# Performance work log

Measured on AMD Instinct MI355X. Metric: run time of the kernel, lower is better.

Reference implementation:

```python
import jax, jax.numpy as jnp
from jax import lax
import numpy as np

B, H, W = 16, 512, 512
OPENING_R, EROSION_R, DILATION_R = 5, 2, 1
MIN_SIZE, AREA_THRESHOLD = 2000, 300
INF = np.int32(2 ** 30)


def _disk(r):
    # skimage.morphology.disk: x^2 + y^2 <= r^2 on a (2r+1)^2 grid
    y, x = np.mgrid[-r:r + 1, -r:r + 1]
    return jnp.asarray((x * x + y * y <= r * r).astype(np.float32))


D_OPEN, D_ERODE, D_DILATE = _disk(OPENING_R), _disk(EROSION_R), _disk(DILATION_R)


def _conv2(x, k):
    return lax.conv_general_dilated(x[None, None], k[None, None], (1, 1), 'VALID')[0, 0]


def _erode(fg, se):
    # skimage binary_erosion uses border_value=True (image border does not erode)
    r = se.shape[0] // 2
    x = jnp.pad(fg.astype(jnp.float32), r, constant_values=1.0)
    return _conv2(x, se) >= se.sum() - 0.5


def _dilate(fg, se):
    # skimage binary_dilation uses border_value=False
    r = se.shape[0] // 2
    x = jnp.pad(fg.astype(jnp.float32), r, constant_values=0.0)
    return _conv2(x, se) > 0.5


def _seg_cummin(v, reset, axis, reverse):
    # segmented cumulative-min: scan resets wherever `reset` is True (background)
    def comb(a, b):
        av, af = a
        bv, bf = b
        return jnp.where(bf, bv, jnp.minimum(av, bv)), af | bf

    vv, _ = lax.associative_scan(comb, (v, reset), axis=axis, reverse=reverse)
    return vv


def _label(fg):
    # 4-connectivity connected-component labeling via min-label propagation.
    # Each fg pixel starts with its raveled index; alternating row/col segmented
    # cummin sweeps run under while_loop until a fixed point (root id per comp).
    h, w = fg.shape
    idx = jnp.arange(h * w, dtype=jnp.int32).reshape(h, w)
    lab0 = jnp.where(fg, idx, INF)
    bg = ~fg

    def sweep(l):
        for axis in (1, 0):
            for rev in (False, True):
                l = jnp.where(fg, _seg_cummin(l, bg, axis, rev), INF)
        return l

    def body(c):
        l, _ = c
        nl = sweep(l)
        return nl, jnp.array_equal(nl, l)

    lab, _ = lax.while_loop(lambda c: ~c[1], body, (lab0, jnp.array(False)))
    seg = jnp.where(fg, lab, 0).ravel()
    sizes = jax.ops.segment_sum(fg.astype(jnp.int32).ravel(), seg, num_segments=h * w)
    ncomp = jnp.sum(sizes > 0)
    return lab, sizes, ncomp


def _remove_small_objects(fg, min_size, guard):
    lab, sizes, ncomp = _label(fg)
    px = sizes[jnp.where(fg, lab, 0)]  # component size at every fg pixel
    kept = fg & (px >= min_size)
    # original only removes small objects when label(...).max() > 1
    return jnp.where(ncomp > 1, kept, fg) if guard else kept


def _pipeline(mask):
    fg = mask > 0
    fg = _remove_small_objects(fg, MIN_SIZE, True)
    # remove_small_holes == ~remove_small_objects(~fg, area_threshold + 1)
    fg = ~_remove_small_objects(~fg, AREA_THRESHOLD + 1, False)
    fg = _erode(fg, D_ERODE)
    fg = _dilate(_erode(fg, D_OPEN), D_OPEN)  # binary_opening
    fg = _remove_small_objects(fg, MIN_SIZE, True)
    fg = _dilate(fg, D_DILATE)
    return fg.astype(jnp.float32)  # original casts to int; float32 kept for vjp parity


def setup_inputs() -> dict:
    key = jax.random.key(0)
    # blobby binary masks: threshold bilinearly-upsampled low-res noise so that
    # realistic large connected components (> min_size px) exist
    low = jax.random.uniform(key, (B, H // 16, W // 16), dtype=jnp.float32)
    blob = jax.image.resize(low, (B, H, W), method='bilinear')
    return {'inputs': (blob > 0.5).astype(jnp.float32)}


def reference(inputs):
    return jax.vmap(_pipeline)(inputs)
```

## Files before the change

kernel.cpp:

```cpp
#include <hip/hip_runtime.h>
#include <stdint.h>

#define BATCH 16
#define H 512
#define W 512
#define HW (H * W)
#define NTOT (BATCH * HW)
#define NWORDS (NTOT / 64)

#define SROWS 16
#define SWORDS 128
#define SPIX 8192
#define NSTRIPS (NWORDS / SWORDS)
#define IMG_STRIPS 32
#define NBOUND_IMG 248

#define MAXR 4096
#define NR (NSTRIPS * MAXR)

#define SPIN_LIMIT (1 << 20)

__device__ __forceinline__ int ald(const int* p) {
    return __hip_atomic_load((int*)p, __ATOMIC_RELAXED, __HIP_MEMORY_SCOPE_AGENT);
}
__device__ __forceinline__ void ast(int* p, int v) {
    __hip_atomic_store(p, v, __ATOMIC_RELAXED, __HIP_MEMORY_SCOPE_AGENT);
}
__device__ __forceinline__ uint64_t ald64(const uint64_t* p) {
    return __hip_atomic_load((uint64_t*)p, __ATOMIC_RELAXED, __HIP_MEMORY_SCOPE_AGENT);
}
__device__ __forceinline__ void ast64(uint64_t* p, uint64_t v) {
    __hip_atomic_store(p, v, __ATOMIC_RELAXED, __HIP_MEMORY_SCOPE_AGENT);
}

__device__ __forceinline__ int find_root_c(int* L, int x) {
    int r = x, p = ald(&L[r]);
    while (p != r) { r = p; p = ald(&L[r]); }
    if (ald(&L[x]) != r) atomicMin(&L[x], r);
    return r;
}

__device__ void merge_uf(int* L, int a, int b) {
    while (true) {
        a = find_root_c(L, a);
        b = find_root_c(L, b);
        if (a == b) return;
        int lo = a < b ? a : b;
        int hi = a < b ? b : a;
        int old = atomicMin(&L[hi], lo);
        if (old == hi) return;
        a = lo; b = old;
    }
}

__device__ __forceinline__ int find_root_lds(int* P, int x) {
    int r = x, p = P[r];
    while (p != r) { r = p; p = P[r]; }
    return r;
}

__device__ void merge_lds(int* P, int a, int b) {
    while (true) {
        a = find_root_lds(P, a);
        b = find_root_lds(P, b);
        if (a == b) return;
        int lo = a < b ? a : b;
        int hi = a < b ? b : a;
        int old = atomicMin(&P[hi], lo);
        if (old == hi) return;
        a = lo; b = old;
    }
}

__device__ __forceinline__ int run_of(uint64_t m, int i, int cvrid, int wr) {
    uint64_t below = i ? ((~m) & ((1ull << i) - 1)) : 0ull;
    if (below == 0) return (cvrid >= 0) ? cvrid : wr;
    int s = 64 - __builtin_clzll(below);
    uint64_t starts = m & ~((m << 1) | ((cvrid >= 0) ? 1ull : 0ull));
    return wr + __popcll(starts & ((1ull << s) - 1));
}

__device__ __forceinline__ int run_of_lds(uint64_t m, int i, int cvrid,
                                          uint64_t starts, int wb) {
    uint64_t below = i ? ((~m) & ((1ull << i) - 1)) : 0ull;
    if (below == 0) return (cvrid >= 0) ? cvrid : wb;
    int s = 64 - __builtin_clzll(below);
    return wb + __popcll(starts & ((1ull << s) - 1));
}

__device__ uint64_t keep_word(const uint64_t* __restrict__ bits,
                              const int* __restrict__ carry, const int* __restrict__ wordrun,
                              const int* __restrict__ L, const int* __restrict__ sizes,
                              const int* __restrict__ ncomp, int minsz, int gw) {
    uint64_t m = ald64(&bits[gw]);
    uint64_t res = m;
    if (m && ald(&ncomp[gw >> 12]) > 1) {
        int cv = ald(&carry[gw]);
        int wr = ald(&wordrun[gw]);
        int rk = 0;
        while (m) {
            int s = __builtin_ctzll(m);
            uint64_t rest = m >> s;
            uint64_t nr = ~rest;
            int len = nr ? __builtin_ctzll(nr) : (64 - s);
            uint64_t piece = ((len >= 64) ? ~0ull : ((1ull << len) - 1)) << s;
            bool initial = !(s == 0 && cv >= 0);
            int rid = initial ? (wr + rk++) : cv;
            if (ald(&sizes[ald(&L[rid])]) < minsz) res &= ~piece;
            m &= ~piece;
        }
    }
    return res;
}

__device__ uint64_t fill_word(const uint64_t* __restrict__ bits,
                              const int* __restrict__ carry, const int* __restrict__ wordrun,
                              const int* __restrict__ L, const int* __restrict__ sizes,
                              int minsz, int gw) {
    uint64_t fg = ald64(&bits[gw]);
    uint64_t bg = ~fg;
    uint64_t res = fg;
    int cv = ald(&carry[gw]);
    int wr = ald(&wordrun[gw]);
    int rk = 0;
    while (bg) {
        int s = __builtin_ctzll(bg);
        uint64_t rest = bg >> s;
        uint64_t nr = ~rest;
        int len = nr ? __builtin_ctzll(nr) : (64 - s);
        uint64_t piece = ((len >= 64) ? ~0ull : ((1ull << len) - 1)) << s;
        bool initial = !(s == 0 && cv >= 0);
        int rid = initial ? (wr + rk++) : cv;
        if (ald(&sizes[ald(&L[rid])]) < minsz) res |= piece;
        bg &= ~piece;
    }
    return res;
}

template <int R, bool ERODE>
__device__ uint64_t morph_word_lds(const uint64_t* buf, int lrow, int w, int gyTop) {
    const uint64_t BORDER = ERODE ? ~0ull : 0ull;
    uint64_t res = ERODE ? ~0ull : 0ull;
#pragma unroll
    for (int dy = -R; dy <= R; ++dy) {
        int lr = lrow + dy;
        int gy = gyTop + lr;
        if (gy < 0 || gy >= H) continue;
        int v = R * R - dy * dy;
        int kx = 0;
        while ((kx + 1) * (kx + 1) <= v) ++kx;
        uint64_t cur = buf[lr * 8 + w];
        uint64_t prv = (w > 0) ? buf[lr * 8 + w - 1] : BORDER;
        uint64_t nxt = (w < 7) ? buf[lr * 8 + w + 1] : BORDER;
        uint64_t acc = cur;
#pragma unroll
        for (int dx = 1; dx <= kx; ++dx) {
            uint64_t right = (cur >> dx) | (nxt << (64 - dx));
            uint64_t left  = (cur << dx) | (prv >> (64 - dx));
            if (ERODE) acc &= right & left;
            else       acc |= right | left;
        }
        if (ERODE) res &= acc;
        else       res |= acc;
    }
    return res;
}

__device__ void strip_ccl_body(uint64_t m, uint64_t* sw, int* scarry,
                               int* cntL, int* wbL, int* par,
                               int blk, int t,
                               int* __restrict__ carry, int* __restrict__ wordrun,
                               int* __restrict__ L, int* __restrict__ sizes,
                               int* __restrict__ ncomp) {
    if (t < SWORDS) sw[t] = m;
    __syncthreads();

    if (t < SWORDS) {
        bool cont = (t & 7) ? ((sw[t - 1] >> 63) != 0) : false;
        int c = __popcll(m & ~(m << 1));
        if ((m & 1ull) && cont) --c;
        cntL[t] = c;
        wbL[t] = c;
    }
    __syncthreads();
    for (int off = 1; off < SWORDS; off <<= 1) {
        int v = 0;
        if (t < SWORDS && t >= off) v = wbL[t - off];
        __syncthreads();
        if (t < SWORDS) wbL[t] += v;
        __syncthreads();
    }

    if (t < SROWS) {
        int cv = -1;
        for (int i = 0; i < 8; ++i) {
            int lw = t * 8 + i;
            scarry[lw] = cv;
            uint64_t w = sw[lw];
            if (w >> 63) { if (cntL[lw] > 0) cv = wbL[lw] - 1; }
            else cv = -1;
        }
    }
    for (int i = t; i < MAXR; i += 256) par[i] = i;
    __syncthreads();

    int cv = -1, wb = 0;
    uint64_t starts = 0ull;
    if (t < SWORDS) {
        cv = scarry[t];
        wb = wbL[t] - cntL[t];
        ast(&carry[blk * SWORDS + t], (cv >= 0) ? (blk * MAXR + cv) : -1);
        ast(&wordrun[blk * SWORDS + t], blk * MAXR + wb);
        starts = m & ~((m << 1) | ((cv >= 0) ? 1ull : 0ull));
    }
    __syncthreads();

    if (t >= 8 && t < SWORDS && m) {
        uint64_t up = sw[t - 8];
        uint64_t cand = m & up;
        if (cand) {
            uint64_t curprev = (t & 7) ? sw[t - 1] : 0ull;
            uint64_t upprev  = (t & 7) ? sw[t - 9] : 0ull;
            uint64_t curl = (m << 1) | (curprev >> 63);
            uint64_t upl  = (up << 1) | (upprev >> 63);
            cand &= ~(curl & upl);
            int cvu = scarry[t - 8];
            int wbu = wbL[t - 8] - cntL[t - 8];
            uint64_t startsU = up & ~((up << 1) | ((cvu >= 0) ? 1ull : 0ull));
            while (cand) {
                int i = __builtin_ctzll(cand);
                int sP = run_of_lds(m, i, cv, starts, wb);
                int sQ = run_of_lds(up, i, cvu, startsU, wbu);
                merge_lds(par, sP, sQ);
                cand &= cand - 1;
            }
        }
    }
    __syncthreads();

    if (t < SWORDS) {
        int g = blk * MAXR;
        uint64_t ss = starts;
        int rk = 0;
        while (ss) {
            int rid = wb + rk; ++rk;
            int r = find_root_lds(par, rid);
            ast(&L[g + rid], g + r);
            if (r == rid) ast(&sizes[g + rid], 0);
            ss &= ss - 1;
        }
    }
    if (t == 0 && (blk & 31) == 0) ast(&ncomp[blk >> 5], 0);
}

__device__ void merge_bound_item(const uint64_t* __restrict__ bits, uint64_t inv64,
                                 const int* __restrict__ carry,
                                 const int* __restrict__ wordrun,
                                 int* __restrict__ L, int gw, int w) {
    uint64_t cur = ald64(&bits[gw]) ^ inv64;
    uint64_t up  = ald64(&bits[gw - 8]) ^ inv64;
    uint64_t cand = cur & up;
    if (!cand) return;
    uint64_t curprev = w ? (ald64(&bits[gw - 1]) ^ inv64) : 0ull;
    uint64_t upprev  = w ? (ald64(&bits[gw - 9]) ^ inv64) : 0ull;
    uint64_t curl = (cur << 1) | (curprev >> 63);
    uint64_t upl  = (up << 1)  | (upprev >> 63);
    cand &= ~(curl & upl);
    if (!cand) return;
    int cvc = ald(&carry[gw]), cvu = ald(&carry[gw - 8]);
    int wrc = ald(&wordrun[gw]), wru = ald(&wordrun[gw - 8]);
    while (cand) {
        int i = __builtin_ctzll(cand);
        int sP = run_of(cur, i, cvc, wrc);
        int sQ = run_of(up, i, cvu, wru);
        merge_uf(L, sP, sQ);
        cand &= cand - 1;
    }
}

__device__ void flatten_block(const uint64_t* __restrict__ bits, uint64_t inv64,
                              const int* __restrict__ carry,
                              const int* __restrict__ wordrun,
                              int* __restrict__ L,
                              int* __restrict__ sizes, int* __restrict__ ncomp,
                              int blk, int t, int* hk, int* hv) {
    if (t < 128) { hk[t] = -1; hv[t] = 0; }
    __syncthreads();
    if (t < SWORDS) {
        int gw = blk * SWORDS + t;
        uint64_t m = ald64(&bits[gw]) ^ inv64;
        if (m) {
            int cv = ald(&carry[gw]);
            int wr = ald(&wordrun[gw]);
            int rk = 0;
            while (m) {
                int s = __builtin_ctzll(m);
                uint64_t rest = m >> s;
                uint64_t nr = ~rest;
                int len = nr ? __builtin_ctzll(nr) : (64 - s);
                uint64_t piece = ((len >= 64) ? ~0ull : ((1ull << len) - 1)) << s;
                bool initial = !(s == 0 && cv >= 0);
                int rid = initial ? (wr + rk++) : cv;
                int r = find_root_c(L, rid);
                if (initial && r == rid) atomicAdd(&ncomp[gw >> 12], 1);
                int cnt = __popcll(piece);
                uint32_t h = ((uint32_t)r * 2654435761u) >> 25;
                bool done = false;
                for (int tt = 0; tt < 16; ++tt) {
                    int slot = (h + tt) & 127;
                    int k = hk[slot];
                    if (k == -1) k = atomicCAS(&hk[slot], -1, r);
                    if (k == -1 || k == r) { atomicAdd(&hv[slot], cnt); done = true; break; }
                }
                if (!done) atomicAdd(&sizes[r], cnt);
                m &= ~piece;
            }
        }
    }
    __syncthreads();
    if (t < 128 && hk[t] != -1) atomicAdd(&sizes[hk[t]], hv[t]);
}

__device__ void keep_dilate_seg(const uint64_t* __restrict__ bits,
                                const int* __restrict__ carry,
                                const int* __restrict__ wordrun,
                                const int* __restrict__ L,
                                const int* __restrict__ sizes,
                                const int* __restrict__ ncomp,
                                float* __restrict__ out,
                                int img, int y0, int t, uint64_t* kb, uint64_t* db) {
    if (t < 80) {
        int lr = t >> 3;
        int w = t & 7;
        int gy = y0 - 1 + lr;
        uint64_t v = 0;
        if (gy >= 0 && gy < H)
            v = keep_word(bits, carry, wordrun, L, sizes, ncomp, 2000,
                          img * 4096 + gy * 8 + w);
        kb[t] = v;
    }
    __syncthreads();
    if (t < 64) {
        int r = t >> 3, w = t & 7;
        uint64_t cur = kb[(r + 1) * 8 + w];
        uint64_t up  = kb[r * 8 + w];
        uint64_t dn  = kb[(r + 2) * 8 + w];
        uint64_t prv = w ? kb[(r + 1) * 8 + w - 1] : 0ull;
        uint64_t nxt = (w < 7) ? kb[(r + 1) * 8 + w + 1] : 0ull;
        db[t] = cur | up | dn | (cur << 1) | (prv >> 63) | (cur >> 1) | (nxt << 63);
    }
    __syncthreads();

    int q0 = t * 16;
    uint64_t wd = db[q0 >> 6];
    int sh = q0 & 63;
    float4* o = (float4*)(out + (size_t)img * HW + (size_t)y0 * W + q0);
#pragma unroll
    for (int k = 0; k < 4; ++k) {
        uint32_t nib = (uint32_t)(wd >> (sh + k * 4)) & 0xFu;
        float4 f;
        f.x = (nib & 1u) ? 1.0f : 0.0f;
        f.y = (nib & 2u) ? 1.0f : 0.0f;
        f.z = (nib & 4u) ? 1.0f : 0.0f;
        f.w = (nib & 8u) ? 1.0f : 0.0f;
        o[k] = f;
    }
}

__device__ __forceinline__ void ibar(int* flags, int img, int si, int phase) {
    int* base = flags + img * 32;
    __syncthreads();
    if (threadIdx.x == 0) {
        asm volatile("s_waitcnt vmcnt(0)" ::: "memory");
        ast(&base[si], phase);
    }
    if (threadIdx.x < 32) {
        int spins = 0;
        while (ald(&base[threadIdx.x]) < phase && ++spins < SPIN_LIMIT)
            __builtin_amdgcn_s_sleep(1);
    }
    __syncthreads();
}

__global__ __launch_bounds__(256, 2) void k_mega(
        const float4* __restrict__ in4, float* __restrict__ out,
        int* LA, int* sizesA, int* LB, int* sizesB,
        uint64_t* bits1, uint64_t* bits2, uint64_t* bits3,
        int* carryA, int* carryB, int* wordrunA, int* wordrunB,
        int* ncompA, int* ncompB, int* flags) {
    __shared__ uint64_t sw[SWORDS];
    __shared__ int scarry[SWORDS];
    __shared__ int cntL[SWORDS];
    __shared__ int wbL[SWORDS];
    __shared__ union US {
        int par[MAXR];
        struct { uint64_t A[320]; uint64_t B[320]; } mo;
        struct { int hk[128]; int hv[128]; } ha;
        struct { uint64_t kb[80]; uint64_t db[64]; } kd;
    } U;
    int blk = blockIdx.x;
    int t = threadIdx.x;
    int img = blk >> 5, si = blk & 31;

#pragma unroll
    for (int it = 0; it < 8; ++it) {
        int q = blk * (SPIX / 4) + it * 256 + t;
        float4 v = in4[q];
        uint32_t nib = (v.x > 0.0f ? 1u : 0u) | (v.y > 0.0f ? 2u : 0u) |
                       (v.z > 0.0f ? 4u : 0u) | (v.w > 0.0f ? 8u : 0u);
        uint64_t val = (uint64_t)nib << (4 * (t & 15));
        val |= __shfl_xor(val, 1);
        val |= __shfl_xor(val, 2);
        val |= __shfl_xor(val, 4);
        val |= __shfl_xor(val, 8);
        if ((t & 15) == 0) ast64(&bits1[q >> 4], val);
    }
    __syncthreads();

    {
        uint64_t m = (t < SWORDS) ? ald64(&bits1[blk * SWORDS + t]) : 0ull;
        strip_ccl_body(m, sw, scarry, cntL, wbL, U.par, blk, t,
                       carryA, wordrunA, LA, sizesA, ncompA);
    }
    ibar(flags, img, si, 1);

    if (t < 8) {
        int item = si * 8 + t;
        if (item < NBOUND_IMG) {
            int gw = img * 4096 + ((item >> 3) + 1) * SROWS * 8 + (item & 7);
            merge_bound_item(bits1, 0ull, carryA, wordrunA, LA, gw, item & 7);
        }
    }
    ibar(flags, img, si, 2);

    flatten_block(bits1, 0ull, carryA, wordrunA, LA, sizesA, ncompA,
                  blk, t, U.ha.hk, U.ha.hv);
    ibar(flags, img, si, 3);

    {
        uint64_t m = 0ull;
        if (t < SWORDS) {
            int gw = blk * SWORDS + t;
            uint64_t kw = keep_word(bits1, carryA, wordrunA, LA, sizesA, ncompA,
                                    2000, gw);
            ast64(&bits2[gw], kw);
            m = ~kw;
        }
        strip_ccl_body(m, sw, scarry, cntL, wbL, U.par, blk, t,
                       carryB, wordrunB, LB, sizesB, ncompB);
    }
    ibar(flags, img, si, 4);

    if (t < 8) {
        int item = si * 8 + t;
        if (item < NBOUND_IMG) {
            int gw = img * 4096 + ((item >> 3) + 1) * SROWS * 8 + (item & 7);
            merge_bound_item(bits2, ~0ull, carryB, wordrunB, LB, gw, item & 7);
        }
    }
    ibar(flags, img, si, 5);

    flatten_block(bits2, ~0ull, carryB, wordrunB, LB, sizesB, ncompB,
                  blk, t, U.ha.hk, U.ha.hv);
    ibar(flags, img, si, 6);

    {
        int gyTop = si * 16 - 12;
        for (int lw = t; lw < 320; lw += 256) {
            int gy = gyTop + (lw >> 3);
            int w = lw & 7;
            uint64_t v = 0;
            if (gy >= 0 && gy < H)
                v = fill_word(bits2, carryB, wordrunB, LB, sizesB, 301,
                              img * 4096 + gy * 8 + w);
            U.mo.A[lw] = v;
        }
        __syncthreads();
        for (int lw = t; lw < 320; lw += 256) {
            int lr = lw >> 3;
            if (lr >= 2 && lr <= 37) U.mo.B[lw] = morph_word_lds<2, true>(U.mo.A, lr, lw & 7, gyTop);
        }
        __syncthreads();
        for (int lw = t; lw < 320; lw += 256) {
            int lr = lw >> 3;
            if (lr >= 7 && lr <= 32) U.mo.A[lw] = morph_word_lds<5, true>(U.mo.B, lr, lw & 7, gyTop);
        }
        __syncthreads();
        for (int lw = t; lw < 320; lw += 256) {
            int lr = lw >> 3;
            if (lr >= 12 && lr <= 27) U.mo.B[lw] = morph_word_lds<5, false>(U.mo.A, lr, lw & 7, gyTop);
        }
        __syncthreads();
        uint64_t m3 = 0ull;
        if (t < SWORDS) {
            m3 = U.mo.B[t + 96];
            ast64(&bits3[blk * SWORDS + t], m3);
        }
        strip_ccl_body(m3, sw, scarry, cntL, wbL, U.par, blk, t,
                       carryA, wordrunA, LA, sizesA, ncompA);
    }
    ibar(flags, img, si, 7);

    if (t < 8) {
        int item = si * 8 + t;
        if (item < NBOUND_IMG) {
            int gw = img * 4096 + ((item >> 3) + 1) * SROWS * 8 + (item & 7);
            merge_bound_item(bits3, 0ull, carryA, wordrunA, LA, gw, item & 7);
        }
    }
    ibar(flags, img, si, 8);

    flatten_block(bits3, 0ull, carryA, wordrunA, LA, sizesA, ncompA,
                  blk, t, U.ha.hk, U.ha.hv);
    ibar(flags, img, si, 9);

    for (int k = 0; k < 2; ++k) {
        int seg = blk * 2 + k;
        int s8 = seg & 63;
        keep_dilate_seg(bits3, carryA, wordrunA, LA, sizesA, ncompA, out,
                        img, s8 * 8, t, U.kd.kb, U.kd.db);
        __syncthreads();
    }
}

extern "C" void kernel_launch(void* const* d_in, const int* in_sizes, int n_in,
                              void* d_out, int out_size, void* d_ws, size_t ws_size,
                              hipStream_t stream) {
    const float* in = (const float*)d_in[0];
    float* out = (float*)d_out;

    uint8_t* ws = (uint8_t*)d_ws;
    int* LA      = (int*)ws;
    int* sizesA  = LA + NR;
    int* LB      = sizesA + NR;
    int* sizesB  = LB + NR;
    uint64_t* bits1 = (uint64_t*)(sizesB + NR);
    uint64_t* bits2 = bits1 + NWORDS;
    uint64_t* bits3 = bits2 + NWORDS;
    int* carryA   = (int*)(bits3 + NWORDS);
    int* carryB   = carryA + NWORDS;
    int* wordrunA = carryB + NWORDS;
    int* wordrunB = wordrunA + NWORDS;
    int* ncompA   = wordrunB + NWORDS;
    int* ncompB   = ncompA + BATCH;
    int* flags    = ncompB + BATCH;

    hipMemsetAsync(flags, 0, BATCH * 32 * sizeof(int), stream);

    k_mega<<<NSTRIPS, 256, 0, stream>>>((const float4*)in, out,
                                        LA, sizesA, LB, sizesB,
                                        bits1, bits2, bits3,
                                        carryA, carryB, wordrunA, wordrunB,
                                        ncompA, ncompB, flags);
}
```

Before: 186.9 us.

## Reuse strip-local LDS CCL state, batch label lookups, and drop flag memset via epochs

Boundary merge, flatten, keep and fill steps now read the strip's own words, carries and run bases from shared memory instead of reloading them from global memory. Root and size lookups for the first four runs of each word are issued together to expose memory-level parallelism. The per-launch memset of the barrier flags is replaced by a persistent device array with epoch-relative phases, removing one extra launch. This relies on the shared-memory state still holding the matching stage's data at each step, and it makes the barrier flags grow monotonically across calls.

```diff
diff --git a/kernel.cpp b/kernel.cpp
--- a/kernel.cpp
+++ b/kernel.cpp
@@ -13,12 +13,13 @@
 #define SPIX 8192
 #define NSTRIPS (NWORDS / SWORDS)
 #define IMG_STRIPS 32
-#define NBOUND_IMG 248
 
 #define MAXR 4096
 #define NR (NSTRIPS * MAXR)
 
 #define SPIN_LIMIT (1 << 20)
+
+__device__ int g_flags[BATCH * 32];
 
 __device__ __forceinline__ int ald(const int* p) {
     return __hip_atomic_load((int*)p, __ATOMIC_RELAXED, __HIP_MEMORY_SCOPE_AGENT);
@@ -88,53 +89,179 @@
     return wb + __popcll(starts & ((1ull << s) - 1));
 }
 
-__device__ uint64_t keep_word(const uint64_t* __restrict__ bits,
-                              const int* __restrict__ carry, const int* __restrict__ wordrun,
-                              const int* __restrict__ L, const int* __restrict__ sizes,
-                              const int* __restrict__ ncomp, int minsz, int gw) {
-    uint64_t m = ald64(&bits[gw]);
+__device__ __forceinline__ void hash_add(int* hk, int* hv, int* sizes,
+                                         int r, int cnt) {
+    uint32_t h = ((uint32_t)r * 2654435761u) >> 25;
+    for (int tt = 0; tt < 16; ++tt) {
+        int slot = (h + tt) & 127;
+        int k = hk[slot];
+        if (k == -1) k = atomicCAS(&hk[slot], -1, r);
+        if (k == -1 || k == r) { atomicAdd(&hv[slot], cnt); return; }
+    }
+    atomicAdd(&sizes[r], cnt);
+}
+
+__device__ uint64_t keep_core(uint64_t m, int cvg, int wrg, int nc,
+                              const int* L, const int* sizes, int minsz) {
     uint64_t res = m;
-    if (m && ald(&ncomp[gw >> 12]) > 1) {
-        int cv = ald(&carry[gw]);
-        int wr = ald(&wordrun[gw]);
-        int rk = 0;
-        while (m) {
-            int s = __builtin_ctzll(m);
-            uint64_t rest = m >> s;
+    if (!m) return res;
+    uint64_t rem = m;
+    uint64_t pc[4]; int rd[4];
+    int rk = 0;
+#pragma unroll
+    for (int k = 0; k < 4; ++k) {
+        pc[k] = 0; rd[k] = wrg;
+        if (rem) {
+            int s = __builtin_ctzll(rem);
+            uint64_t rest = rem >> s;
             uint64_t nr = ~rest;
             int len = nr ? __builtin_ctzll(nr) : (64 - s);
             uint64_t piece = ((len >= 64) ? ~0ull : ((1ull << len) - 1)) << s;
-            bool initial = !(s == 0 && cv >= 0);
-            int rid = initial ? (wr + rk++) : cv;
+            bool initial = !(s == 0 && cvg >= 0);
+            pc[k] = piece;
+            rd[k] = initial ? (wrg + rk) : cvg;
+            rk += initial ? 1 : 0;
+            rem &= ~piece;
+        }
+    }
+    int rt[4], sz[4];
+#pragma unroll
+    for (int k = 0; k < 4; ++k) rt[k] = ald(&L[rd[k]]);
+#pragma unroll
+    for (int k = 0; k < 4; ++k) {
+        int idx = pc[k] ? rt[k] : rd[k];
+        sz[k] = ald(&sizes[idx]);
+    }
+    if (nc > 1) {
+#pragma unroll
+        for (int k = 0; k < 4; ++k)
+            if (pc[k] && sz[k] < minsz) res &= ~pc[k];
+        while (rem) {
+            int s = __builtin_ctzll(rem);
+            uint64_t rest = rem >> s;
+            uint64_t nr = ~rest;
+            int len = nr ? __builtin_ctzll(nr) : (64 - s);
+            uint64_t piece = ((len >= 64) ? ~0ull : ((1ull << len) - 1)) << s;
+            int rid = wrg + rk++;
             if (ald(&sizes[ald(&L[rid])]) < minsz) res &= ~piece;
-            m &= ~piece;
+            rem &= ~piece;
         }
     }
     return res;
 }
 
-__device__ uint64_t fill_word(const uint64_t* __restrict__ bits,
-                              const int* __restrict__ carry, const int* __restrict__ wordrun,
-                              const int* __restrict__ L, const int* __restrict__ sizes,
-                              int minsz, int gw) {
-    uint64_t fg = ald64(&bits[gw]);
+__device__ uint64_t fill_core(uint64_t fg, int cvg, int wrg,
+                              const int* L, const int* sizes, int minsz) {
     uint64_t bg = ~fg;
     uint64_t res = fg;
-    int cv = ald(&carry[gw]);
-    int wr = ald(&wordrun[gw]);
+    if (!bg) return res;
+    uint64_t rem = bg;
+    uint64_t pc[4]; int rd[4];
     int rk = 0;
-    while (bg) {
-        int s = __builtin_ctzll(bg);
-        uint64_t rest = bg >> s;
+#pragma unroll
+    for (int k = 0; k < 4; ++k) {
+        pc[k] = 0; rd[k] = wrg;
+        if (rem) {
+            int s = __builtin_ctzll(rem);
+            uint64_t rest = rem >> s;
+            uint64_t nr = ~rest;
+            int len = nr ? __builtin_ctzll(nr) : (64 - s);
+            uint64_t piece = ((len >= 64) ? ~0ull : ((1ull << len) - 1)) << s;
+            bool initial = !(s == 0 && cvg >= 0);
+            pc[k] = piece;
+            rd[k] = initial ? (wrg + rk) : cvg;
+            rk += initial ? 1 : 0;
+            rem &= ~piece;
+        }
+    }
+    int rt[4], sz[4];
+#pragma unroll
+    for (int k = 0; k < 4; ++k) rt[k] = ald(&L[rd[k]]);
+#pragma unroll
+    for (int k = 0; k < 4; ++k) {
+        int idx = pc[k] ? rt[k] : rd[k];
+        sz[k] = ald(&sizes[idx]);
+    }
+#pragma unroll
+    for (int k = 0; k < 4; ++k)
+        if (pc[k] && sz[k] < minsz) res |= pc[k];
+    while (rem) {
+        int s = __builtin_ctzll(rem);
+        uint64_t rest = rem >> s;
         uint64_t nr = ~rest;
         int len = nr ? __builtin_ctzll(nr) : (64 - s);
         uint64_t piece = ((len >= 64) ? ~0ull : ((1ull << len) - 1)) << s;
-        bool initial = !(s == 0 && cv >= 0);
-        int rid = initial ? (wr + rk++) : cv;
+        int rid = wrg + rk++;
         if (ald(&sizes[ald(&L[rid])]) < minsz) res |= piece;
-        bg &= ~piece;
+        rem &= ~piece;
     }
     return res;
+}
+
+__device__ void flatten_fast(uint64_t m, int cvg, int wrg,
+                             int* L, int* sizes, int* ncomp_img,
+                             int t, int* hk, int* hv) {
+    if (t < 128) { hk[t] = -1; hv[t] = 0; }
+    __syncthreads();
+    if (t < SWORDS && m) {
+        uint64_t rem = m;
+        uint64_t pc[4]; int rd[4]; bool ini[4];
+        int rk = 0;
+#pragma unroll
+        for (int k = 0; k < 4; ++k) {
+            pc[k] = 0; rd[k] = wrg; ini[k] = false;
+            if (rem) {
+                int s = __builtin_ctzll(rem);
+                uint64_t rest = rem >> s;
+                uint64_t nr = ~rest;
+                int len = nr ? __builtin_ctzll(nr) : (64 - s);
+                uint64_t piece = ((len >= 64) ? ~0ull : ((1ull << len) - 1)) << s;
+                bool initial = !(s == 0 && cvg >= 0);
+                pc[k] = piece;
+                rd[k] = initial ? (wrg + rk) : cvg;
+                ini[k] = initial;
+                rk += initial ? 1 : 0;
+                rem &= ~piece;
+            }
+        }
+        int h1[4], h2[4];
+#pragma unroll
+        for (int k = 0; k < 4; ++k) h1[k] = ald(&L[rd[k]]);
+#pragma unroll
+        for (int k = 0; k < 4; ++k) {
+            int i1 = pc[k] ? h1[k] : rd[k];
+            h2[k] = ald(&L[i1]);
+        }
+#pragma unroll
+        for (int k = 0; k < 4; ++k) {
+            if (pc[k]) {
+                int r;
+                if (h2[k] == h1[k]) r = h1[k];
+                else {
+                    r = h2[k];
+                    int p = ald(&L[r]);
+                    while (p != r) { r = p; p = ald(&L[r]); }
+                }
+                if (h1[k] != r) atomicMin(&L[rd[k]], r);
+                if (ini[k] && r == rd[k]) atomicAdd(ncomp_img, 1);
+                hash_add(hk, hv, sizes, r, __popcll(pc[k]));
+            }
+        }
+        while (rem) {
+            int s = __builtin_ctzll(rem);
+            uint64_t rest = rem >> s;
+            uint64_t nr = ~rest;
+            int len = nr ? __builtin_ctzll(nr) : (64 - s);
+            uint64_t piece = ((len >= 64) ? ~0ull : ((1ull << len) - 1)) << s;
+            int rid = wrg + rk++;
+            int r = find_root_c(L, rid);
+            if (r == rid) atomicAdd(ncomp_img, 1);
+            hash_add(hk, hv, sizes, r, __popcll(piece));
+            rem &= ~piece;
+        }
+    }
+    __syncthreads();
+    if (t < 128 && hk[t] != -1) atomicAdd(&sizes[hk[t]], hv[t]);
 }
 
 template <int R, bool ERODE>
@@ -253,130 +380,16 @@
     if (t == 0 && (blk & 31) == 0) ast(&ncomp[blk >> 5], 0);
 }
 
-__device__ void merge_bound_item(const uint64_t* __restrict__ bits, uint64_t inv64,
-                                 const int* __restrict__ carry,
-                                 const int* __restrict__ wordrun,
-                                 int* __restrict__ L, int gw, int w) {
-    uint64_t cur = ald64(&bits[gw]) ^ inv64;
-    uint64_t up  = ald64(&bits[gw - 8]) ^ inv64;
-    uint64_t cand = cur & up;
-    if (!cand) return;
-    uint64_t curprev = w ? (ald64(&bits[gw - 1]) ^ inv64) : 0ull;
-    uint64_t upprev  = w ? (ald64(&bits[gw - 9]) ^ inv64) : 0ull;
-    uint64_t curl = (cur << 1) | (curprev >> 63);
-    uint64_t upl  = (up << 1)  | (upprev >> 63);
-    cand &= ~(curl & upl);
-    if (!cand) return;
-    int cvc = ald(&carry[gw]), cvu = ald(&carry[gw - 8]);
-    int wrc = ald(&wordrun[gw]), wru = ald(&wordrun[gw - 8]);
-    while (cand) {
-        int i = __builtin_ctzll(cand);
-        int sP = run_of(cur, i, cvc, wrc);
-        int sQ = run_of(up, i, cvu, wru);
-        merge_uf(L, sP, sQ);
-        cand &= cand - 1;
-    }
-}
-
-__device__ void flatten_block(const uint64_t* __restrict__ bits, uint64_t inv64,
-                              const int* __restrict__ carry,
-                              const int* __restrict__ wordrun,
-                              int* __restrict__ L,
-                              int* __restrict__ sizes, int* __restrict__ ncomp,
-                              int blk, int t, int* hk, int* hv) {
-    if (t < 128) { hk[t] = -1; hv[t] = 0; }
-    __syncthreads();
-    if (t < SWORDS) {
-        int gw = blk * SWORDS + t;
-        uint64_t m = ald64(&bits[gw]) ^ inv64;
-        if (m) {
-            int cv = ald(&carry[gw]);
-            int wr = ald(&wordrun[gw]);
-            int rk = 0;
-            while (m) {
-                int s = __builtin_ctzll(m);
-                uint64_t rest = m >> s;
-                uint64_t nr = ~rest;
-                int len = nr ? __builtin_ctzll(nr) : (64 - s);
-                uint64_t piece = ((len >= 64) ? ~0ull : ((1ull << len) - 1)) << s;
-                bool initial = !(s == 0 && cv >= 0);
-                int rid = initial ? (wr + rk++) : cv;
-                int r = find_root_c(L, rid);
-                if (initial && r == rid) atomicAdd(&ncomp[gw >> 12], 1);
-                int cnt = __popcll(piece);
-                uint32_t h = ((uint32_t)r * 2654435761u) >> 25;
-                bool done = false;
-                for (int tt = 0; tt < 16; ++tt) {
-                    int slot = (h + tt) & 127;
-                    int k = hk[slot];
-                    if (k == -1) k = atomicCAS(&hk[slot], -1, r);
-                    if (k == -1 || k == r) { atomicAdd(&hv[slot], cnt); done = true; break; }
-                }
-                if (!done) atomicAdd(&sizes[r], cnt);
-                m &= ~piece;
-            }
-        }
-    }
-    __syncthreads();
-    if (t < 128 && hk[t] != -1) atomicAdd(&sizes[hk[t]], hv[t]);
-}
-
-__device__ void keep_dilate_seg(const uint64_t* __restrict__ bits,
-                                const int* __restrict__ carry,
-                                const int* __restrict__ wordrun,
-                                const int* __restrict__ L,
-                                const int* __restrict__ sizes,
-                                const int* __restrict__ ncomp,
-                                float* __restrict__ out,
-                                int img, int y0, int t, uint64_t* kb, uint64_t* db) {
-    if (t < 80) {
-        int lr = t >> 3;
-        int w = t & 7;
-        int gy = y0 - 1 + lr;
-        uint64_t v = 0;
-        if (gy >= 0 && gy < H)
-            v = keep_word(bits, carry, wordrun, L, sizes, ncomp, 2000,
-                          img * 4096 + gy * 8 + w);
-        kb[t] = v;
-    }
-    __syncthreads();
-    if (t < 64) {
-        int r = t >> 3, w = t & 7;
-        uint64_t cur = kb[(r + 1) * 8 + w];
-        uint64_t up  = kb[r * 8 + w];
-        uint64_t dn  = kb[(r + 2) * 8 + w];
-        uint64_t prv = w ? kb[(r + 1) * 8 + w - 1] : 0ull;
-        uint64_t nxt = (w < 7) ? kb[(r + 1) * 8 + w + 1] : 0ull;
-        db[t] = cur | up | dn | (cur << 1) | (prv >> 63) | (cur >> 1) | (nxt << 63);
-    }
-    __syncthreads();
-
-    int q0 = t * 16;
-    uint64_t wd = db[q0 >> 6];
-    int sh = q0 & 63;
-    float4* o = (float4*)(out + (size_t)img * HW + (size_t)y0 * W + q0);
-#pragma unroll
-    for (int k = 0; k < 4; ++k) {
-        uint32_t nib = (uint32_t)(wd >> (sh + k * 4)) & 0xFu;
-        float4 f;
-        f.x = (nib & 1u) ? 1.0f : 0.0f;
-        f.y = (nib & 2u) ? 1.0f : 0.0f;
-        f.z = (nib & 4u) ? 1.0f : 0.0f;
-        f.w = (nib & 8u) ? 1.0f : 0.0f;
-        o[k] = f;
-    }
-}
-
-__device__ __forceinline__ void ibar(int* flags, int img, int si, int phase) {
-    int* base = flags + img * 32;
+__device__ __forceinline__ void ibar(int img, int si, int ep, int phase) {
+    int* base = g_flags + img * 32;
     __syncthreads();
     if (threadIdx.x == 0) {
         asm volatile("s_waitcnt vmcnt(0)" ::: "memory");
-        ast(&base[si], phase);
+        ast(&base[si], ep + phase);
     }
     if (threadIdx.x < 32) {
         int spins = 0;
-        while (ald(&base[threadIdx.x]) < phase && ++spins < SPIN_LIMIT)
+        while (ald(&base[threadIdx.x]) - ep < phase && ++spins < SPIN_LIMIT)
             __builtin_amdgcn_s_sleep(1);
     }
     __syncthreads();
@@ -387,7 +400,7 @@
         int* LA, int* sizesA, int* LB, int* sizesB,
         uint64_t* bits1, uint64_t* bits2, uint64_t* bits3,
         int* carryA, int* carryB, int* wordrunA, int* wordrunB,
-        int* ncompA, int* ncompB, int* flags) {
+        int* ncompA, int* ncompB) {
     __shared__ uint64_t sw[SWORDS];
     __shared__ int scarry[SWORDS];
     __shared__ int cntL[SWORDS];
@@ -401,6 +414,7 @@
     int blk = blockIdx.x;
     int t = threadIdx.x;
     int img = blk >> 5, si = blk & 31;
+    int ep = ald(&g_flags[img * 32 + si]);
 
 #pragma unroll
     for (int it = 0; it < 8; ++it) {
@@ -413,56 +427,108 @@
         val |= __shfl_xor(val, 2);
         val |= __shfl_xor(val, 4);
         val |= __shfl_xor(val, 8);
-        if ((t & 15) == 0) ast64(&bits1[q >> 4], val);
+        if ((t & 15) == 0) {
+            ast64(&bits1[q >> 4], val);
+            sw[it * 16 + (t >> 4)] = val;
+        }
     }
     __syncthreads();
 
     {
-        uint64_t m = (t < SWORDS) ? ald64(&bits1[blk * SWORDS + t]) : 0ull;
+        uint64_t m = (t < SWORDS) ? sw[t] : 0ull;
         strip_ccl_body(m, sw, scarry, cntL, wbL, U.par, blk, t,
                        carryA, wordrunA, LA, sizesA, ncompA);
     }
-    ibar(flags, img, si, 1);
-
-    if (t < 8) {
-        int item = si * 8 + t;
-        if (item < NBOUND_IMG) {
-            int gw = img * 4096 + ((item >> 3) + 1) * SROWS * 8 + (item & 7);
-            merge_bound_item(bits1, 0ull, carryA, wordrunA, LA, gw, item & 7);
-        }
-    }
-    ibar(flags, img, si, 2);
-
-    flatten_block(bits1, 0ull, carryA, wordrunA, LA, sizesA, ncompA,
-                  blk, t, U.ha.hk, U.ha.hv);
-    ibar(flags, img, si, 3);
+    ibar(img, si, ep, 1);
+
+    if (t < 8 && si < 31) {
+        int gw = (blk + 1) * SWORDS + t;
+        uint64_t cur = ald64(&bits1[gw]);
+        uint64_t curprev = t ? ald64(&bits1[gw - 1]) : 0ull;
+        int cvc = ald(&carryA[gw]);
+        int wrc = ald(&wordrunA[gw]);
+        uint64_t up = sw[120 + t];
+        uint64_t upprev = t ? sw[119 + t] : 0ull;
+        int cvuL = scarry[120 + t];
+        int cvu = cvuL >= 0 ? blk * MAXR + cvuL : -1;
+        int wru = blk * MAXR + (wbL[120 + t] - cntL[120 + t]);
+        uint64_t cand = cur & up;
+        if (cand) {
+            uint64_t curl = (cur << 1) | (curprev >> 63);
+            uint64_t upl  = (up << 1) | (upprev >> 63);
+            cand &= ~(curl & upl);
+            while (cand) {
+                int i = __builtin_ctzll(cand);
+                int sP = run_of(cur, i, cvc, wrc);
+                int sQ = run_of(up, i, cvu, wru);
+                merge_uf(LA, sP, sQ);
+                cand &= cand - 1;
+            }
+        }
+    }
+    ibar(img, si, ep, 2);
 
     {
-        uint64_t m = 0ull;
+        uint64_t m = (t < SWORDS) ? sw[t] : 0ull;
+        int cvL = (t < SWORDS) ? scarry[t] : -1;
+        int cvg = cvL >= 0 ? blk * MAXR + cvL : -1;
+        int wrg = blk * MAXR + ((t < SWORDS) ? (wbL[t] - cntL[t]) : 0);
+        flatten_fast(m, cvg, wrg, LA, sizesA, &ncompA[img], t, U.ha.hk, U.ha.hv);
+    }
+    ibar(img, si, ep, 3);
+
+    {
+        uint64_t m2 = 0ull;
         if (t < SWORDS) {
-            int gw = blk * SWORDS + t;
-            uint64_t kw = keep_word(bits1, carryA, wordrunA, LA, sizesA, ncompA,
-                                    2000, gw);
-            ast64(&bits2[gw], kw);
-            m = ~kw;
-        }
-        strip_ccl_body(m, sw, scarry, cntL, wbL, U.par, blk, t,
+            int nc = ald(&ncompA[img]);
+            uint64_t m1 = sw[t];
+            int cvL = scarry[t];
+            int cvg = cvL >= 0 ? blk * MAXR + cvL : -1;
+            int wrg = blk * MAXR + (wbL[t] - cntL[t]);
+            uint64_t kw = keep_core(m1, cvg, wrg, nc, LA, sizesA, 2000);
+            ast64(&bits2[blk * SWORDS + t], kw);
+            m2 = ~kw;
+        }
+        strip_ccl_body(m2, sw, scarry, cntL, wbL, U.par, blk, t,
                        carryB, wordrunB, LB, sizesB, ncompB);
     }
-    ibar(flags, img, si, 4);
-
-    if (t < 8) {
-        int item = si * 8 + t;
-        if (item < NBOUND_IMG) {
-            int gw = img * 4096 + ((item >> 3) + 1) * SROWS * 8 + (item & 7);
-            merge_bound_item(bits2, ~0ull, carryB, wordrunB, LB, gw, item & 7);
-        }
-    }
-    ibar(flags, img, si, 5);
-
-    flatten_block(bits2, ~0ull, carryB, wordrunB, LB, sizesB, ncompB,
-                  blk, t, U.ha.hk, U.ha.hv);
-    ibar(flags, img, si, 6);
+    ibar(img, si, ep, 4);
+
+    if (t < 8 && si < 31) {
+        int gw = (blk + 1) * SWORDS + t;
+        uint64_t cur = ~ald64(&bits2[gw]);
+        uint64_t curprev = t ? ~ald64(&bits2[gw - 1]) : 0ull;
+        int cvc = ald(&carryB[gw]);
+        int wrc = ald(&wordrunB[gw]);
+        uint64_t up = sw[120 + t];
+        uint64_t upprev = t ? sw[119 + t] : 0ull;
+        int cvuL = scarry[120 + t];
+        int cvu = cvuL >= 0 ? blk * MAXR + cvuL : -1;
+        int wru = blk * MAXR + (wbL[120 + t] - cntL[120 + t]);
+        uint64_t cand = cur & up;
+        if (cand) {
+            uint64_t curl = (cur << 1) | (curprev >> 63);
+            uint64_t upl  = (up << 1) | (upprev >> 63);
+            cand &= ~(curl & upl);
+            while (cand) {
+                int i = __builtin_ctzll(cand);
+                int sP = run_of(cur, i, cvc, wrc);
+                int sQ = run_of(up, i, cvu, wru);
+                merge_uf(LB, sP, sQ);
+                cand &= cand - 1;
+            }
+        }
+    }
+    ibar(img, si, ep, 5);
+
+    {
+        uint64_t m = (t < SWORDS) ? sw[t] : 0ull;
+        int cvL = (t < SWORDS) ? scarry[t] : -1;
+        int cvg = cvL >= 0 ? blk * MAXR + cvL : -1;
+        int wrg = blk * MAXR + ((t < SWORDS) ? (wbL[t] - cntL[t]) : 0);
+        flatten_fast(m, cvg, wrg, LB, sizesB, &ncompB[img], t, U.ha.hk, U.ha.hv);
+    }
+    ibar(img, si, ep, 6);
 
     {
         int gyTop = si * 16 - 12;
@@ -470,9 +536,22 @@
             int gy = gyTop + (lw >> 3);
             int w = lw & 7;
             uint64_t v = 0;
-            if (gy >= 0 && gy < H)
-                v = fill_word(bits2, carryB, wordrunB, LB, sizesB, 301,
-                              img * 4096 + gy * 8 + w);
+            if (gy >= 0 && gy < H) {
+                uint64_t fg; int cvg, wrg;
+                if (lw >= 96 && lw < 224) {
+                    int ti = lw - 96;
+                    fg = ~sw[ti];
+                    int cvL = scarry[ti];
+                    cvg = cvL >= 0 ? blk * MAXR + cvL : -1;
+                    wrg = blk * MAXR + (wbL[ti] - cntL[ti]);
+                } else {
+                    int gw = img * 4096 + gy * 8 + w;
+                    fg = ald64(&bits2[gw]);
+                    cvg = ald(&carryB[gw]);
+                    wrg = ald(&wordrunB[gw]);
+                }
+                v = fill_core(fg, cvg, wrg, LB, sizesB, 301);
+            }
             U.mo.A[lw] = v;
         }
         __syncthreads();
@@ -499,26 +578,99 @@
         strip_ccl_body(m3, sw, scarry, cntL, wbL, U.par, blk, t,
                        carryA, wordrunA, LA, sizesA, ncompA);
     }
-    ibar(flags, img, si, 7);
-
-    if (t < 8) {
-        int item = si * 8 + t;
-        if (item < NBOUND_IMG) {
-            int gw = img * 4096 + ((item >> 3) + 1) * SROWS * 8 + (item & 7);
-            merge_bound_item(bits3, 0ull, carryA, wordrunA, LA, gw, item & 7);
-        }
-    }
-    ibar(flags, img, si, 8);
-
-    flatten_block(bits3, 0ull, carryA, wordrunA, LA, sizesA, ncompA,
-                  blk, t, U.ha.hk, U.ha.hv);
-    ibar(flags, img, si, 9);
+    ibar(img, si, ep, 7);
+
+    if (t < 8 && si < 31) {
+        int gw = (blk + 1) * SWORDS + t;
+        uint64_t cur = ald64(&bits3[gw]);
+        uint64_t curprev = t ? ald64(&bits3[gw - 1]) : 0ull;
+        int cvc = ald(&carryA[gw]);
+        int wrc = ald(&wordrunA[gw]);
+        uint64_t up = sw[120 + t];
+        uint64_t upprev = t ? sw[119 + t] : 0ull;
+        int cvuL = scarry[120 + t];
+        int cvu = cvuL >= 0 ? blk * MAXR + cvuL : -1;
+        int wru = blk * MAXR + (wbL[120 + t] - cntL[120 + t]);
+        uint64_t cand = cur & up;
+        if (cand) {
+            uint64_t curl = (cur << 1) | (curprev >> 63);
+            uint64_t upl  = (up << 1) | (upprev >> 63);
+            cand &= ~(curl & upl);
+            while (cand) {
+                int i = __builtin_ctzll(cand);
+                int sP = run_of(cur, i, cvc, wrc);
+                int sQ = run_of(up, i, cvu, wru);
+                merge_uf(LA, sP, sQ);
+                cand &= cand - 1;
+            }
+        }
+    }
+    ibar(img, si, ep, 8);
+
+    {
+        uint64_t m = (t < SWORDS) ? sw[t] : 0ull;
+        int cvL = (t < SWORDS) ? scarry[t] : -1;
+        int cvg = cvL >= 0 ? blk * MAXR + cvL : -1;
+        int wrg = blk * MAXR + ((t < SWORDS) ? (wbL[t] - cntL[t]) : 0);
+        flatten_fast(m, cvg, wrg, LA, sizesA, &ncompA[img], t, U.ha.hk, U.ha.hv);
+    }
+    ibar(img, si, ep, 9);
 
     for (int k = 0; k < 2; ++k) {
-        int seg = blk * 2 + k;
-        int s8 = seg & 63;
-        keep_dilate_seg(bits3, carryA, wordrunA, LA, sizesA, ncompA, out,
-                        img, s8 * 8, t, U.kd.kb, U.kd.db);
+        int s8 = 2 * si + k;
+        int y0 = s8 * 8;
+        if (t < 80) {
+            int lr = t >> 3, w = t & 7;
+            int gy = y0 - 1 + lr;
+            uint64_t v = 0;
+            if (gy >= 0 && gy < H) {
+                int nc = ald(&ncompA[img]);
+                uint64_t m; int cvg, wrg;
+                int rel = gy - 16 * si;
+                if (rel >= 0 && rel < 16) {
+                    int ti = rel * 8 + w;
+                    m = sw[ti];
+                    int cvL = scarry[ti];
+                    cvg = cvL >= 0 ? blk * MAXR + cvL : -1;
+                    wrg = blk * MAXR + (wbL[ti] - cntL[ti]);
+                } else {
+                    int gw = img * 4096 + gy * 8 + w;
+                    m = ald64(&bits3[gw]);
+                    cvg = ald(&carryA[gw]);
+                    wrg = ald(&wordrunA[gw]);
+                }
+                v = keep_core(m, cvg, wrg, nc, LA, sizesA, 2000);
+            }
+            U.kd.kb[t] = v;
+        }
+        __syncthreads();
+        if (t < 64) {
+            int r = t >> 3, w = t & 7;
+            uint64_t cur = U.kd.kb[(r + 1) * 8 + w];
+            uint64_t up  = U.kd.kb[r * 8 + w];
+            uint64_t dn  = U.kd.kb[(r + 2) * 8 + w];
+            uint64_t prv = w ? U.kd.kb[(r + 1) * 8 + w - 1] : 0ull;
+            uint64_t nxt = (w < 7) ? U.kd.kb[(r + 1) * 8 + w + 1] : 0ull;
+            U.kd.db[t] = cur | up | dn | (cur << 1) | (prv >> 63) |
+                         (cur >> 1) | (nxt << 63);
+        }
+        __syncthreads();
+        {
+            int q0 = t * 16;
+            uint64_t wd = U.kd.db[q0 >> 6];
+            int sh = q0 & 63;
+            float4* o = (float4*)(out + (size_t)img * HW + (size_t)y0 * W + q0);
+#pragma unroll
+            for (int kk = 0; kk < 4; ++kk) {
+                uint32_t nib = (uint32_t)(wd >> (sh + kk * 4)) & 0xFu;
+                float4 f;
+                f.x = (nib & 1u) ? 1.0f : 0.0f;
+                f.y = (nib & 2u) ? 1.0f : 0.0f;
+                f.z = (nib & 4u) ? 1.0f : 0.0f;
+                f.w = (nib & 8u) ? 1.0f : 0.0f;
+                o[kk] = f;
+            }
+        }
         __syncthreads();
     }
 }
@@ -543,13 +695,10 @@
     int* wordrunB = wordrunA + NWORDS;
     int* ncompA   = wordrunB + NWORDS;
     int* ncompB   = ncompA + BATCH;
-    int* flags    = ncompB + BATCH;
-
-    hipMemsetAsync(flags, 0, BATCH * 32 * sizeof(int), stream);
 
     k_mega<<<NSTRIPS, 256, 0, stream>>>((const float4*)in, out,
                                         LA, sizesA, LB, sizesB,
                                         bits1, bits2, bits3,
                                         carryA, carryB, wordrunA, wordrunB,
-                                        ncompA, ncompB, flags);
-}
+                                        ncompA, ncompB);
+}
```

Result: no change. 189.8 us (+1.5%).
